# Kernel optimization log

Measured on AMD Instinct MI355X. Metric: run time of the kernel, lower is better.

Reference implementation:

```python
import jax, jax.numpy as jnp
import numpy as np

B, C_IN, N = 8, 3, 4096
H = [64, 128, 256]      # local conv widths
G = [128, 64]           # global MLP widths
K = 16                  # kNN neighbors for edge_conv
EPS = 1e-5


def _ln(x, g, b):
    # LayerNorm(num_point): normalize over the last (point) axis per channel
    mu = jnp.mean(x, axis=-1, keepdims=True)
    var = jnp.mean((x - mu) ** 2, axis=-1, keepdims=True)
    return (x - mu) / jnp.sqrt(var + EPS) * g + b


def _conv_ln_relu(x, w, b, g, be):
    # 1x1 Conv1d == per-point matmul: [B,Cin,N] -> [B,Cout,N]
    x = jnp.einsum('oi,bin->bon', w, x) + b[None, :, None]
    return jax.nn.relu(_ln(x, g, be))


def _edge_conv(x):
    # DGCNN-style edge conv: kNN in feature space, max-aggregate neighbor feats
    f = jnp.swapaxes(x, 1, 2)                                  # [B,N,C]
    sq = jnp.sum(f * f, axis=-1)                               # [B,N]
    d = sq[:, :, None] + sq[:, None, :] - 2.0 * jnp.einsum('bnc,bmc->bnm', f, f)
    _, idx = jax.lax.top_k(-jax.lax.stop_gradient(d), K)       # [B,N,K]
    nbr = jax.vmap(lambda fb, ib: fb[ib])(f, idx)              # [B,N,K,C] gather
    return jnp.swapaxes(jnp.max(nbr, axis=2), 1, 2)            # [B,C,N]


def setup_inputs() -> dict:
    key = jax.random.key(0)
    ks = jax.random.split(key, 20)
    inp = {"point_cloud": jax.random.normal(ks[0], (B, C_IN, N), jnp.float32)}
    prev = C_IN
    for i, h in enumerate(H):
        inp[f"w{i}"] = jax.random.normal(ks[1 + 3 * i], (h, prev), jnp.float32) * (1.0 / np.sqrt(prev))
        inp[f"b{i}"] = jnp.zeros((h,), jnp.float32)
        inp[f"g{i}"] = jnp.ones((N,), jnp.float32)
        inp[f"be{i}"] = jnp.zeros((N,), jnp.float32)
        prev = h
    for i, h in enumerate(G + [1]):
        inp[f"gw{i}"] = jax.random.normal(ks[10 + i], (h, prev), jnp.float32) * (1.0 / np.sqrt(prev))
        inp[f"gb{i}"] = jnp.zeros((h,), jnp.float32)
        prev = h
    return inp


def reference(point_cloud, w0, b0, g0, be0, w1, b1, g1, be1, w2, b2, g2, be2,
              gw0, gb0, gw1, gb1, gw2, gb2):
    x = _conv_ln_relu(point_cloud, w0, b0, g0, be0)
    x = _conv_ln_relu(x, w1, b1, g1, be1)
    x = _conv_ln_relu(x, w2, b2, g2, be2)
    x = _edge_conv(x)                      # [B,256,N]
    pooled = jnp.mean(x, axis=2)           # mean over points (pnt_axis=2)
    h = jax.nn.relu(pooled @ gw0.T + gb0)
    h = jax.nn.relu(h @ gw1.T + gb1)
    return h @ gw2.T + gb2                 # [B,1] energy
```

## Files before the change

kernel.cpp:

```cpp
#include <hip/hip_runtime.h>
#include <stdint.h>

#define NPTS 4096
#define BATCH 8
#define KNN 16

typedef __attribute__((ext_vector_type(8))) short short8;
typedef __attribute__((ext_vector_type(4))) float f32x4;
typedef unsigned long long u64;

template<int CIN, int G>
__global__ __launch_bounds__(256) void conv_ln_kernel(
    const float* __restrict__ X, const float* __restrict__ W,
    const float* __restrict__ bias, const float* __restrict__ g,
    const float* __restrict__ be, float* __restrict__ Y, int cout) {
    __shared__ float rows[G * NPTS];
    __shared__ double sh[256], sh2[256];
    int b = blockIdx.x;
    int co0 = blockIdx.y * G;
    int t = threadIdx.x;
    const float* xb = X + (size_t)b * CIN * NPTS;

#pragma unroll 1
    for (int chunk = 0; chunk < 4; ++chunk) {
        int n = chunk * 1024 + t * 4;
        f32x4 acc[G];
#pragma unroll
        for (int j = 0; j < G; ++j) {
            float bj = bias[co0 + j];
            acc[j] = (f32x4){bj, bj, bj, bj};
        }
        for (int ci = 0; ci < CIN; ++ci) {
            f32x4 xv = *(const f32x4*)(xb + (size_t)ci * NPTS + n);
#pragma unroll
            for (int j = 0; j < G; ++j) {
                float w = W[(co0 + j) * CIN + ci];
                acc[j].x = fmaf(w, xv.x, acc[j].x);
                acc[j].y = fmaf(w, xv.y, acc[j].y);
                acc[j].z = fmaf(w, xv.z, acc[j].z);
                acc[j].w = fmaf(w, xv.w, acc[j].w);
            }
        }
#pragma unroll
        for (int j = 0; j < G; ++j)
            *(f32x4*)(rows + j * NPTS + n) = acc[j];
    }
    __syncthreads();

#pragma unroll 1
    for (int j = 0; j < G; ++j) {
        float* row = rows + j * NPTS;
        double s = 0.0, s2 = 0.0;
        for (int i = t * 4; i < NPTS; i += 1024) {
            f32x4 v = *(const f32x4*)(row + i);
            s += (double)v.x + (double)v.y + (double)v.z + (double)v.w;
            s2 += (double)v.x * v.x + (double)v.y * v.y
                + (double)v.z * v.z + (double)v.w * v.w;
        }
        sh[t] = s; sh2[t] = s2;
        __syncthreads();
        for (int off = 128; off > 0; off >>= 1) {
            if (t < off) { sh[t] += sh[t + off]; sh2[t] += sh2[t + off]; }
            __syncthreads();
        }
        double mu = sh[0] / (double)NPTS;
        double var = sh2[0] / (double)NPTS - mu * mu;
        float rstd = (float)(1.0 / sqrt(var + 1e-5));
        float muf = (float)mu;
        float* yrow = Y + ((size_t)b * cout + co0 + j) * NPTS;
        for (int i = t * 4; i < NPTS; i += 1024) {
            f32x4 v = *(const f32x4*)(row + i);
            f32x4 gg = *(const f32x4*)(g + i);
            f32x4 bb = *(const f32x4*)(be + i);
            f32x4 o;
            o.x = fmaxf((v.x - muf) * rstd * gg.x + bb.x, 0.f);
            o.y = fmaxf((v.y - muf) * rstd * gg.y + bb.y, 0.f);
            o.z = fmaxf((v.z - muf) * rstd * gg.z + bb.z, 0.f);
            o.w = fmaxf((v.w - muf) * rstd * gg.w + bb.w, 0.f);
            *(f32x4*)(yrow + i) = o;
        }
        __syncthreads();
    }
}

#define ROW_E 72
#define ROW_B 144

__device__ inline unsigned short f2bf_rne(float x) {
    union { float f; unsigned u; } v; v.f = x;
    unsigned u = v.u;
    return (unsigned short)((u + 0x7FFFu + ((u >> 16) & 1u)) >> 16);
}

__global__ __launch_bounds__(256) void convert_kernel(
    const float* __restrict__ X2, unsigned short* __restrict__ Fc,
    float* __restrict__ SQ, float* __restrict__ Xt) {
    __shared__ float T[64][65];
    __shared__ float Q[64][4];
    int b = blockIdx.y;
    int n0 = blockIdx.x * 64;
    int t = threadIdx.x;
    int n_loc = t >> 2, cq = t & 3;
    int wave = t >> 6, lane = t & 63;
    float sacc = 0.f;
    for (int cc = 0; cc < 4; ++cc) {
        for (int r = 0; r < 16; ++r) {
            int cl = r * 4 + (t >> 6);
            T[cl][t & 63] = X2[((size_t)b * 256 + cc * 64 + cl) * NPTS + n0 + (t & 63)];
        }
        __syncthreads();
        if (Xt) {
#pragma unroll
            for (int r = 0; r < 16; ++r) {
                int n_l = wave * 16 + r;
                Xt[((size_t)b * NPTS + n0 + n_l) * 256 + cc * 64 + lane] = T[lane][n_l];
            }
        }
        size_t base = (((size_t)(b * 4 + cc) * NPTS) + n0 + n_loc) * ROW_E;
#pragma unroll
        for (int j = 0; j < 16; ++j) {
            int c = cq * 16 + j;
            float x = T[c][n_loc];
            sacc = fmaf(x, x, sacc);
            Fc[base + c] = f2bf_rne(x);
        }
        __syncthreads();
    }
    Q[n_loc][cq] = sacc;
    __syncthreads();
    if (t < 64)
        SQ[(size_t)b * NPTS + n0 + t] = Q[t][0] + Q[t][1] + Q[t][2] + Q[t][3];
}

#define A_BYTES 18432
#define BUF_B   36864
#define SENT32 0xFFFFFFFFu

__device__ inline void async_cp16(const void* g, void* l) {
    __builtin_amdgcn_global_load_lds((const __attribute__((address_space(1))) void*)g,
                                     (__attribute__((address_space(3))) void*)l, 16, 0, 0);
}

__device__ inline unsigned flip_f(float d) {
    union { float f; unsigned u; } v; v.f = d;
    return v.u ^ (((unsigned)((int)v.u >> 31)) | 0x80000000u);
}
__device__ inline float unflip_f(unsigned y) {
    unsigned m = (~((unsigned)((int)y >> 31))) | 0x80000000u;
    union { unsigned u; float f; } v; v.u = y ^ m;
    return v.f;
}
__device__ inline float thr_of(unsigned p) {
    unsigned tb = p | 0xFFFu;
    if (tb >= 0xFF800000u) tb = 0xFF800000u;
    return unflip_f(tb);
}

__global__ __launch_bounds__(256) void knn_mfma_kernel(
    const unsigned short* __restrict__ Fc, const float* __restrict__ SQ,
    unsigned* __restrict__ DpA, unsigned* __restrict__ DpB) {
    __shared__ __align__(16) char smem[2 * BUF_B];
    __shared__ float sq_ks[128];
    __shared__ float thrx[256];
    int b = blockIdx.x;
    int q0 = blockIdx.y * 128;
    int ks = blockIdx.z;
    int t = threadIdx.x;
    int lane = t & 63;
    int wv = t >> 6;
    int wq = wv & 1, wk = wv >> 1;
    int quad = lane >> 4;
    int l15 = lane & 15;
    const float* sqb = SQ + (size_t)b * NPTS;
    const char* FcB = (const char*)Fc + (size_t)b * 4 * NPTS * ROW_B;

    thrx[t] = __int_as_float(0x7F800000);

    unsigned lst[KNN];
#pragma unroll
    for (int j = 0; j < KNN; ++j) lst[j] = SENT32;
    float thr_part = __int_as_float(0x7F800000);

    int q = t & 127, sub = t >> 7;

    {
        const char* gA = FcB + (size_t)q0 * ROW_B;
        const char* gB = FcB + (size_t)(ks * 1024) * ROW_B;
#pragma unroll
        for (int i = 0; i < 9; ++i) {
            int chunk = (i * 4 + wv) * 1024;
            const char* g = (chunk < A_BYTES) ? (gA + chunk) : (gB + (chunk - A_BYTES));
            async_cp16(g + lane * 16, smem + chunk);
        }
    }
    __syncthreads();

    for (int kt = 0; kt < 8; ++kt) {
        int kbase = ks * 1024 + kt * 128;
        if (t < 128) sq_ks[t] = sqb[kbase + t];
        f32x4 acc[4][4];
#pragma unroll
        for (int i = 0; i < 4; ++i)
#pragma unroll
            for (int j = 0; j < 4; ++j) acc[i][j] = (f32x4){0.f, 0.f, 0.f, 0.f};

#pragma unroll 1
        for (int kc = 0; kc < 4; ++kc) {
            int g = kt * 4 + kc;
            int gn = g + 1;
            if (gn < 32) {
                int kcn = gn & 3, ktn = gn >> 2;
                const char* gA = FcB + ((size_t)kcn * NPTS + q0) * ROW_B;
                const char* gB = FcB + ((size_t)kcn * NPTS + ks * 1024 + ktn * 128) * ROW_B;
                char* dst = smem + (gn & 1) * BUF_B;
#pragma unroll
                for (int i = 0; i < 9; ++i) {
                    int chunk = (i * 4 + wv) * 1024;
                    const char* gp = (chunk < A_BYTES) ? (gA + chunk) : (gB + (chunk - A_BYTES));
                    async_cp16(gp + lane * 16, dst + chunk);
                }
            }
            const char* base = smem + (g & 1) * BUF_B;
#pragma unroll
            for (int kss = 0; kss < 2; ++kss) {
                int coff = kss * 64 + quad * 16;
                short8 a[4], bf[4];
#pragma unroll
                for (int tq = 0; tq < 4; ++tq)
                    a[tq] = *(const short8*)(base + (wq * 64 + tq * 16 + l15) * ROW_B + coff);
#pragma unroll
                for (int tk = 0; tk < 4; ++tk)
                    bf[tk] = *(const short8*)(base + A_BYTES + (wk * 64 + tk * 16 + l15) * ROW_B + coff);
#pragma unroll
                for (int tq = 0; tq < 4; ++tq)
#pragma unroll
                    for (int tk = 0; tk < 4; ++tk)
                        acc[tq][tk] = __builtin_amdgcn_mfma_f32_16x16x32_bf16(
                            a[tq], bf[tk], acc[tq][tk], 0, 0, 0);
            }
            __syncthreads();
        }

        float* Gd = (float*)(smem + BUF_B);
        const float* gq = Gd + (size_t)q * 68 + sub * 32;
#pragma unroll 1
        for (int h = 0; h < 2; ++h) {
            if (wk == h) {
#pragma unroll
                for (int tk = 0; tk < 4; ++tk) {
                    float sqk = sq_ks[h * 64 + tk * 16 + l15];
#pragma unroll
                    for (int tq = 0; tq < 4; ++tq) {
                        float* gp = Gd + (size_t)(wq * 64 + tq * 16 + quad * 4) * 68
                                  + tk * 16 + l15;
                        f32x4 g = acc[tq][tk];
                        gp[0]   = fmaf(-2.f, g.x, sqk);
                        gp[68]  = fmaf(-2.f, g.y, sqk);
                        gp[136] = fmaf(-2.f, g.z, sqk);
                        gp[204] = fmaf(-2.f, g.w, sqk);
                    }
                }
            }
            __syncthreads();
            if (h == 0) thr_part = thrx[t ^ 128];
            float thrf = fminf(thr_of(lst[KNN - 1]), thr_part);
            unsigned mask = 0;
#pragma unroll
            for (int i = 7; i >= 0; --i) {
                f32x4 v = *(const f32x4*)(gq + i * 4);
                mask = mask + mask + (unsigned)(v.w <= thrf);
                mask = mask + mask + (unsigned)(v.z <= thrf);
                mask = mask + mask + (unsigned)(v.y <= thrf);
                mask = mask + mask + (unsigned)(v.x <= thrf);
            }
            while (__any((int)(mask != 0u))) {
                if (mask) {
                    int j = __ffs(mask) - 1;
                    mask &= mask - 1u;
                    float d = gq[j];
                    unsigned pk = (flip_f(d) & 0xFFFFF000u)
                                | (unsigned)(kbase + h * 64 + sub * 32 + j);
                    if (pk < lst[KNN - 1]) {
                        lst[KNN - 1] = pk;
#pragma unroll
                        for (int s = KNN - 1; s > 0; --s) {
                            if (lst[s] < lst[s - 1]) {
                                unsigned tmp = lst[s]; lst[s] = lst[s - 1]; lst[s - 1] = tmp;
                            }
                        }
                    }
                }
            }
            if (h == 1) thrx[t] = thr_of(lst[KNN - 1]);
            __syncthreads();
        }
    }

    unsigned* mls = (unsigned*)smem;
#pragma unroll
    for (int j = 0; j < KNN; ++j) mls[t * 17 + j] = lst[j];
    __syncthreads();
    if (t < 128) {
        const unsigned* da = mls + t * 17;
        const unsigned* db = mls + (t + 128) * 17;
        unsigned* outp = ((ks < 2) ? DpA : DpB)
                       + ((size_t)((b * NPTS + q0 + t) * 2 + (ks & 1))) * KNN;
        int ia = 0, ib2 = 0;
        for (int k = 0; k < KNN; ++k) {
            bool ta = (ib2 >= KNN) || (ia < KNN && da[ia] < db[ib2]);
            outp[k] = ta ? da[ia++] : db[ib2++];
        }
    }
}

__global__ __launch_bounds__(256) void transpose_kernel(
    const float* __restrict__ X2, float* __restrict__ Xt) {
    __shared__ float T[64][65];
    int b = blockIdx.x;
    int n0 = blockIdx.y * 64;
    int t = threadIdx.x;
    int wave = t >> 6, lane = t & 63;
    for (int cc = 0; cc < 4; ++cc) {
        for (int r = 0; r < 16; ++r) {
            int cl = r * 4 + (t >> 6);
            T[cl][t & 63] = X2[((size_t)b * 256 + cc * 64 + cl) * NPTS + n0 + (t & 63)];
        }
        __syncthreads();
#pragma unroll
        for (int r = 0; r < 16; ++r) {
            int n_l = wave * 16 + r;
            Xt[((size_t)b * NPTS + n0 + n_l) * 256 + cc * 64 + lane] = T[lane][n_l];
        }
        __syncthreads();
    }
}

__global__ __launch_bounds__(256) void gather_pool_kernel(
    const float* __restrict__ Xt, const unsigned* __restrict__ DpA,
    const unsigned* __restrict__ DpB, float* __restrict__ Pp) {
    __shared__ int idxs[16][KNN];
    int b = blockIdx.x, blk = blockIdx.y;
    int t = threadIdx.x;
    if (t < 16) {
        int qg = b * NPTS + blk * 16 + t;
        const unsigned* L0 = DpA + (size_t)qg * 2 * KNN;
        const unsigned* L1 = L0 + KNN;
        const unsigned* L2 = DpB + (size_t)qg * 2 * KNN;
        const unsigned* L3 = L2 + KNN;
        int p0 = 0, p1 = 0, p2 = 0, p3 = 0;
#pragma unroll 1
        for (int k = 0; k < KNN; ++k) {
            unsigned v0 = (p0 < KNN) ? L0[p0] : SENT32;
            unsigned v1 = (p1 < KNN) ? L1[p1] : SENT32;
            unsigned v2 = (p2 < KNN) ? L2[p2] : SENT32;
            unsigned v3 = (p3 < KNN) ? L3[p3] : SENT32;
            unsigned best = v0; int bl = 0;
            if (v1 < best) { best = v1; bl = 1; }
            if (v2 < best) { best = v2; bl = 2; }
            if (v3 < best) { best = v3; bl = 3; }
            idxs[t][k] = (int)(best & 0xFFFu);
            if (bl == 0) ++p0; else if (bl == 1) ++p1; else if (bl == 2) ++p2; else ++p3;
        }
    }
    __syncthreads();
    int wv = t >> 6, lane = t & 63;
    const float* xb = Xt + (size_t)b * NPTS * 256;
    f32x4 sum = (f32x4){0.f, 0.f, 0.f, 0.f};
#pragma unroll 1
    for (int i = 0; i < 4; ++i) {
        const int* idp = idxs[wv * 4 + i];
        f32x4 m = *(const f32x4*)(xb + (size_t)idp[0] * 256 + lane * 4);
#pragma unroll
        for (int k = 1; k < KNN; ++k) {
            f32x4 v = *(const f32x4*)(xb + (size_t)idp[k] * 256 + lane * 4);
            m.x = fmaxf(m.x, v.x); m.y = fmaxf(m.y, v.y);
            m.z = fmaxf(m.z, v.z); m.w = fmaxf(m.w, v.w);
        }
        sum.x += m.x; sum.y += m.y; sum.z += m.z; sum.w += m.w;
    }
    __shared__ float S[4][256];
    *(f32x4*)&S[wv][lane * 4] = sum;
    __syncthreads();
    Pp[((size_t)b * 256 + blk) * 256 + t] = S[0][t] + S[1][t] + S[2][t] + S[3][t];
}

__global__ __launch_bounds__(256) void pool_mlp_kernel(
    const float* __restrict__ Pp,
    const float* __restrict__ gw0, const float* __restrict__ gb0,
    const float* __restrict__ gw1, const float* __restrict__ gb1,
    const float* __restrict__ gw2, const float* __restrict__ gb2,
    float* __restrict__ out) {
    __shared__ float P[256];
    __shared__ float h1[128];
    __shared__ float h2[64];
    int b = blockIdx.x, t = threadIdx.x;
    double s = 0.0;
#pragma unroll 4
    for (int j = 0; j < 256; ++j) s += (double)Pp[((size_t)b * 256 + j) * 256 + t];
    P[t] = (float)(s / (double)NPTS);
    __syncthreads();
    if (t < 128) {
        const float* w = gw0 + t * 256;
        double acc = 0.0;
        for (int c = 0; c < 256; ++c) acc += (double)P[c] * (double)w[c];
        float v = gb0[t] + (float)acc;
        h1[t] = v > 0.f ? v : 0.f;
    }
    __syncthreads();
    if (t < 64) {
        const float* w = gw1 + t * 128;
        double acc = 0.0;
        for (int c = 0; c < 128; ++c) acc += (double)h1[c] * (double)w[c];
        float v = gb1[t] + (float)acc;
        h2[t] = v > 0.f ? v : 0.f;
    }
    __syncthreads();
    if (t == 0) {
        double acc = 0.0;
        for (int c = 0; c < 64; ++c) acc += (double)h2[c] * (double)gw2[c];
        out[b] = gb2[0] + (float)acc;
    }
}

extern "C" void kernel_launch(void* const* d_in, const int* in_sizes, int n_in,
                              void* d_out, int out_size, void* d_ws, size_t ws_size,
                              hipStream_t stream) {
    const float* pc  = (const float*)d_in[0];
    const float* w0  = (const float*)d_in[1];
    const float* b0  = (const float*)d_in[2];
    const float* g0  = (const float*)d_in[3];
    const float* be0 = (const float*)d_in[4];
    const float* w1  = (const float*)d_in[5];
    const float* b1  = (const float*)d_in[6];
    const float* g1  = (const float*)d_in[7];
    const float* be1 = (const float*)d_in[8];
    const float* w2  = (const float*)d_in[9];
    const float* b2  = (const float*)d_in[10];
    const float* g2  = (const float*)d_in[11];
    const float* be2 = (const float*)d_in[12];
    const float* gw0 = (const float*)d_in[13];
    const float* gb0 = (const float*)d_in[14];
    const float* gw1 = (const float*)d_in[15];
    const float* gb1 = (const float*)d_in[16];
    const float* gw2 = (const float*)d_in[17];
    const float* gb2 = (const float*)d_in[18];
    float* out = (float*)d_out;

    float* ws = (float*)d_ws;
    float* X0 = ws;
    float* X2 = X0 + 2097152;
    float* R  = X2 + 8388608;
    float* X1 = R;
    unsigned short* Fc = (unsigned short*)R;
    unsigned* DpA = (unsigned*)X0;
    unsigned* DpB = (unsigned*)(R + 9437184);
    float* SQ = R + 11534336;
    float* P  = SQ + 32768;
    float* Pp = P + 2048;
    float* Xt2 = Pp + 524288;

    bool roomy = ws_size >= (size_t)(22579200ull + 8388608ull) * 4ull;
    float* Xt = roomy ? Xt2 : R;

    conv_ln_kernel<3, 2><<<dim3(BATCH, 64 / 2), 256, 0, stream>>>(
        pc, w0, b0, g0, be0, X0, 64);
    conv_ln_kernel<64, 4><<<dim3(BATCH, 128 / 4), 256, 0, stream>>>(
        X0, w1, b1, g1, be1, X1, 128);
    conv_ln_kernel<128, 4><<<dim3(BATCH, 256 / 4), 256, 0, stream>>>(
        X1, w2, b2, g2, be2, X2, 256);

    convert_kernel<<<dim3(NPTS / 64, BATCH), 256, 0, stream>>>(
        X2, Fc, SQ, roomy ? Xt2 : nullptr);
    knn_mfma_kernel<<<dim3(BATCH, 32, 4), 256, 0, stream>>>(Fc, SQ, DpA, DpB);
    if (!roomy)
        transpose_kernel<<<dim3(BATCH, NPTS / 64), 256, 0, stream>>>(X2, Xt);
    gather_pool_kernel<<<dim3(BATCH, 256), 256, 0, stream>>>(Xt, DpA, DpB, Pp);
    pool_mlp_kernel<<<dim3(BATCH), 256, 0, stream>>>(Pp, gw0, gb0, gw1, gb1, gw2, gb2, out);
}
```

Measured before the change: 475.7 us.

## Keep kNN query-tile A fragments resident in registers across key tiles

The query (A) tile fragments for all four channel chunks are preloaded once into registers (afr), so the inner loop only streams and double-buffers the key (B) tile through shared memory. The distance scratch area gets its own LDS region, and launch bounds request two blocks per CU. This removes the repeated global-to-LDS copies and LDS reads of the A tile for every key tile. In exchange it adds 128 VGPRs per thread for the fragments, which could cause spills or limit occupancy, and the kc loop is now fully unrolled.

Result: no change. 477.8 us (+0.5%).

```diff
diff --git a/kernel.cpp b/kernel.cpp
--- a/kernel.cpp
+++ b/kernel.cpp
@@ -132,8 +132,9 @@
         SQ[(size_t)b * NPTS + n0 + t] = Q[t][0] + Q[t][1] + Q[t][2] + Q[t][3];
 }
 
-#define A_BYTES 18432
-#define BUF_B   36864
+#define B_TILE  18432
+#define GD_OFF  (2 * B_TILE)
+#define SMEM_SZ (GD_OFF + 34816)
 #define SENT32 0xFFFFFFFFu
 
 __device__ inline void async_cp16(const void* g, void* l) {
@@ -156,10 +157,10 @@
     return unflip_f(tb);
 }
 
-__global__ __launch_bounds__(256) void knn_mfma_kernel(
+__global__ __launch_bounds__(256, 2) void knn_mfma_kernel(
     const unsigned short* __restrict__ Fc, const float* __restrict__ SQ,
     unsigned* __restrict__ DpA, unsigned* __restrict__ DpB) {
-    __shared__ __align__(16) char smem[2 * BUF_B];
+    __shared__ __align__(16) char smem[SMEM_SZ];
     __shared__ float sq_ks[128];
     __shared__ float thrx[256];
     int b = blockIdx.x;
@@ -183,15 +184,40 @@
 
     int q = t & 127, sub = t >> 7;
 
+    short8 afr[4][2][4];
     {
-        const char* gA = FcB + (size_t)q0 * ROW_B;
+        const char* g0p = FcB + (size_t)q0 * ROW_B;
+#pragma unroll
+        for (int i = 0; i < 4; ++i)
+            async_cp16(g0p + (i * 256 + t) * 16, smem + (i * 256 + t) * 16);
+        if (t < 128) async_cp16(g0p + (1024 + t) * 16, smem + (1024 + t) * 16);
+        __syncthreads();
+#pragma unroll
+        for (int kc = 0; kc < 4; ++kc) {
+            if (kc < 3) {
+                const char* gn = FcB + ((size_t)(kc + 1) * NPTS + q0) * ROW_B;
+                char* d = smem + ((kc + 1) & 1) * B_TILE;
+#pragma unroll
+                for (int i = 0; i < 4; ++i)
+                    async_cp16(gn + (i * 256 + t) * 16, d + (i * 256 + t) * 16);
+                if (t < 128) async_cp16(gn + (1024 + t) * 16, d + (1024 + t) * 16);
+            }
+            const char* Ab = smem + (kc & 1) * B_TILE;
+#pragma unroll
+            for (int kss = 0; kss < 2; ++kss)
+#pragma unroll
+                for (int tq = 0; tq < 4; ++tq)
+                    afr[kc][kss][tq] = *(const short8*)(
+                        Ab + (wq * 64 + tq * 16 + l15) * ROW_B + kss * 64 + quad * 16);
+            __syncthreads();
+        }
+    }
+    {
         const char* gB = FcB + (size_t)(ks * 1024) * ROW_B;
 #pragma unroll
-        for (int i = 0; i < 9; ++i) {
-            int chunk = (i * 4 + wv) * 1024;
-            const char* g = (chunk < A_BYTES) ? (gA + chunk) : (gB + (chunk - A_BYTES));
-            async_cp16(g + lane * 16, smem + chunk);
-        }
+        for (int i = 0; i < 4; ++i)
+            async_cp16(gB + (i * 256 + t) * 16, smem + (i * 256 + t) * 16);
+        if (t < 128) async_cp16(gB + (1024 + t) * 16, smem + (1024 + t) * 16);
     }
     __syncthreads();
 
@@ -204,44 +230,38 @@
 #pragma unroll
             for (int j = 0; j < 4; ++j) acc[i][j] = (f32x4){0.f, 0.f, 0.f, 0.f};
 
-#pragma unroll 1
+#pragma unroll
         for (int kc = 0; kc < 4; ++kc) {
             int g = kt * 4 + kc;
             int gn = g + 1;
             if (gn < 32) {
                 int kcn = gn & 3, ktn = gn >> 2;
-                const char* gA = FcB + ((size_t)kcn * NPTS + q0) * ROW_B;
                 const char* gB = FcB + ((size_t)kcn * NPTS + ks * 1024 + ktn * 128) * ROW_B;
-                char* dst = smem + (gn & 1) * BUF_B;
-#pragma unroll
-                for (int i = 0; i < 9; ++i) {
-                    int chunk = (i * 4 + wv) * 1024;
-                    const char* gp = (chunk < A_BYTES) ? (gA + chunk) : (gB + (chunk - A_BYTES));
-                    async_cp16(gp + lane * 16, dst + chunk);
-                }
-            }
-            const char* base = smem + (g & 1) * BUF_B;
+                char* dst = smem + (gn & 1) * B_TILE;
+#pragma unroll
+                for (int i = 0; i < 4; ++i)
+                    async_cp16(gB + (i * 256 + t) * 16, dst + (i * 256 + t) * 16);
+                if (t < 128) async_cp16(gB + (1024 + t) * 16, dst + (1024 + t) * 16);
+            }
+            const char* base = smem + (g & 1) * B_TILE;
 #pragma unroll
             for (int kss = 0; kss < 2; ++kss) {
                 int coff = kss * 64 + quad * 16;
-                short8 a[4], bf[4];
-#pragma unroll
-                for (int tq = 0; tq < 4; ++tq)
-                    a[tq] = *(const short8*)(base + (wq * 64 + tq * 16 + l15) * ROW_B + coff);
+                short8 bf[4];
 #pragma unroll
                 for (int tk = 0; tk < 4; ++tk)
-                    bf[tk] = *(const short8*)(base + A_BYTES + (wk * 64 + tk * 16 + l15) * ROW_B + coff);
+                    bf[tk] = *(const short8*)(base + (wk * 64 + tk * 16 + l15) * ROW_B + coff);
 #pragma unroll
                 for (int tq = 0; tq < 4; ++tq)
 #pragma unroll
                     for (int tk = 0; tk < 4; ++tk)
                         acc[tq][tk] = __builtin_amdgcn_mfma_f32_16x16x32_bf16(
-                            a[tq], bf[tk], acc[tq][tk], 0, 0, 0);
+                            afr[kc][kss][tq], bf[tk], acc[tq][tk], 0, 0, 0);
             }
             __syncthreads();
         }
 
-        float* Gd = (float*)(smem + BUF_B);
+        float* Gd = (float*)(smem + GD_OFF);
         const float* gq = Gd + (size_t)q * 68 + sub * 32;
 #pragma unroll 1
         for (int h = 0; h < 2; ++h) {
```
